# Kernel tuning notes

Hardware: AMD Instinct MI355X
Metric: run time of the kernel (lower is better)

## Reference

```python
import jax, jax.numpy as jnp
import numpy as np

B, T, C, HD = 4, 4096, 1024, 64  # batch, seq, n_embd, head_dim = n_embd//n_head


def setup_inputs() -> dict:
    key = jax.random.key(0)
    k1, k2, k3, k4 = jax.random.split(key, 4)
    scale = 0.02
    return {
        "x": jax.random.normal(k1, (B, T, C), dtype=jnp.float32),
        "Wq": jax.random.normal(k2, (C, HD), dtype=jnp.float32) * scale,
        "Wk": jax.random.normal(k3, (C, HD), dtype=jnp.float32) * scale,
        "Wv": jax.random.normal(k4, (C, HD), dtype=jnp.float32) * scale,
    }


def reference(x, Wq, Wk, Wv):
    # single-head projections: [B,T,C] @ [C,HD] -> [B,T,HD]
    q = jnp.einsum("btc,ch->bth", x, Wq)
    k = jnp.einsum("btc,ch->bth", x, Wk)
    v = jnp.einsum("btc,ch->bth", x, Wv)
    scale = k.shape[-1] ** -0.5
    # scores: [B,T,T], causal mask via -inf, stable softmax
    alpha = jnp.einsum("bqh,bkh->bqk", q, k) * scale
    t = x.shape[1]
    causal = jnp.tril(jnp.ones((t, t), dtype=bool))
    alpha = jnp.where(causal, alpha, -jnp.inf)
    alpha = jax.nn.softmax(alpha, axis=-1)
    # dropout p=0.0 -> identity
    h = jnp.einsum("bqk,bkh->bqh", alpha, v)
    return h
```

## Files before the change

### kernel.cpp

```cpp
#include <hip/hip_runtime.h>

#define T_SEQ 4096
#define C_DIM 1024
#define HD 64
#define NCH 272

typedef __attribute__((ext_vector_type(8))) __bf16 bf16x8;
typedef __attribute__((ext_vector_type(8))) unsigned short us8;
typedef __attribute__((ext_vector_type(4))) unsigned short us4;
typedef __attribute__((ext_vector_type(4))) float f32x4;
typedef __attribute__((ext_vector_type(16))) float f32x16;

#define QSCALE 0.18033688011112042f

__device__ __forceinline__ unsigned short f2bf(float f) {
    union { float f; unsigned u; } x; x.f = f;
    unsigned r = x.u + 0x7FFFu + ((x.u >> 16) & 1u);
    return (unsigned short)(r >> 16);
}

__device__ __forceinline__ float bf2f(unsigned short u) {
    union { unsigned u; float f; } x; x.u = ((unsigned)u) << 16;
    return x.f;
}

__device__ __forceinline__ us8 cvt8(float4 a, float4 b) {
    union { __bf16 h[8]; us8 v; } u;
    u.h[0] = (__bf16)a.x; u.h[1] = (__bf16)a.y; u.h[2] = (__bf16)a.z; u.h[3] = (__bf16)a.w;
    u.h[4] = (__bf16)b.x; u.h[5] = (__bf16)b.y; u.h[6] = (__bf16)b.z; u.h[7] = (__bf16)b.w;
    return u.v;
}

__device__ __forceinline__ us4 cvt4f(float a, float b, float c, float d) {
    union { __bf16 h[4]; us4 v; } u;
    u.h[0] = (__bf16)a; u.h[1] = (__bf16)b; u.h[2] = (__bf16)c; u.h[3] = (__bf16)d;
    return u.v;
}

__device__ __forceinline__ f32x16 zero16() {
    f32x16 v;
    #pragma unroll
    for (int j = 0; j < 16; ++j) v[j] = 0.f;
    return v;
}

__device__ __forceinline__ void gll16(const unsigned short* g, unsigned short* l) {
    __builtin_amdgcn_global_load_lds(
        (const __attribute__((address_space(1))) unsigned int*)g,
        (__attribute__((address_space(3))) unsigned int*)l,
        16, 0, 0);
}

__device__ __forceinline__ int swzs(int idx) {
    return idx ^ ((((idx) >> 6) & 7) << 3);
}

__device__ __forceinline__ int offf(int qt) {
    const int m = qt >> 1;
    return (qt & 1) ? (m + 1) * (m + 1) : m * m + m;
}

__global__ __launch_bounds__(256) void k_wtrans(const float* __restrict__ Wq,
                                                const float* __restrict__ Wk,
                                                const float* __restrict__ Wv,
                                                unsigned short* __restrict__ wt_g) {
    __shared__ unsigned short tile[64][72];
    const int bx = blockIdx.x;
    const int which = bx >> 4;
    const int kc = bx & 15;
    const int k0 = kc * 64;
    const float* W = (which == 0) ? Wq : ((which == 1) ? Wk : Wv);
    const int t = threadIdx.x;
    {
        const int r = t >> 2, c0 = (t & 3) * 16;
        const float4* src = reinterpret_cast<const float4*>(W + (k0 + r) * HD + c0);
        #pragma unroll
        for (int i = 0; i < 4; ++i) {
            float4 v = src[i];
            tile[r][c0 + 4 * i + 0] = f2bf(v.x);
            tile[r][c0 + 4 * i + 1] = f2bf(v.y);
            tile[r][c0 + 4 * i + 2] = f2bf(v.z);
            tile[r][c0 + 4 * i + 3] = f2bf(v.w);
        }
    }
    __syncthreads();
    {
        const int n = t >> 2, kc0 = (t & 3) * 16;
        alignas(16) unsigned short o[16];
        #pragma unroll
        for (int i = 0; i < 16; ++i) o[i] = tile[kc0 + i][n];
        const int row = which * 64 + n;
        const int g0 = kc0 >> 3;
        unsigned short* base = wt_g + (size_t)kc * 12288 + row * 64;
        *reinterpret_cast<us8*>(base + ((g0 ^ (row & 7)) << 3))       = *reinterpret_cast<const us8*>(&o[0]);
        *reinterpret_cast<us8*>(base + (((g0 + 1) ^ (row & 7)) << 3)) = *reinterpret_cast<const us8*>(&o[8]);
    }
}

__global__ __launch_bounds__(256) void k_proj(const float* __restrict__ x,
                                              const unsigned short* __restrict__ wt_g,
                                              unsigned short* __restrict__ qs,
                                              unsigned short* __restrict__ ksb,
                                              unsigned short* __restrict__ vt) {
    __shared__ unsigned short smem[29184];
    const int tid = threadIdx.x;
    const int w = tid >> 6, lane = tid & 63;
    const int l15 = lane & 15, g = lane >> 4;
    const int m0 = blockIdx.x * 32;
    const int sr = tid >> 3, sc0 = (tid & 7) * 8;
    const float* xrow = x + (size_t)(m0 + sr) * C_DIM + sc0;

    f32x4 acc[3][2];
    #pragma unroll
    for (int mf = 0; mf < 3; ++mf)
        #pragma unroll
        for (int nf = 0; nf < 2; ++nf)
            acc[mf][nf] = (f32x4){0.f, 0.f, 0.f, 0.f};

    {
        float4 xa = *reinterpret_cast<const float4*>(xrow);
        float4 xb = *reinterpret_cast<const float4*>(xrow + 4);
        *reinterpret_cast<us8*>(smem + sr * 72 + sc0) = cvt8(xa, xb);
        const unsigned short* wsrc = wt_g + w * 3072 + lane * 8;
        #pragma unroll
        for (int j = 0; j < 6; ++j)
            gll16(wsrc + j * 512, smem + 4608 + w * 3072 + j * 512);
    }
    __syncthreads();

    for (int kk = 0; kk < 16; ++kk) {
        const int cur = kk & 1;
        const int xb = cur * 2304,  xbn = (cur ^ 1) * 2304;
        const int wb = 4608 + cur * 12288, wbn = 4608 + (cur ^ 1) * 12288;
        float4 na, nb;
        if (kk < 15) {
            const unsigned short* wsrc = wt_g + (size_t)(kk + 1) * 12288 + w * 3072 + lane * 8;
            #pragma unroll
            for (int j = 0; j < 6; ++j)
                gll16(wsrc + j * 512, smem + wbn + w * 3072 + j * 512);
            na = *reinterpret_cast<const float4*>(xrow + (kk + 1) * 64);
            nb = *reinterpret_cast<const float4*>(xrow + (kk + 1) * 64 + 4);
        }
        #pragma unroll
        for (int k2 = 0; k2 < 2; ++k2) {
            bf16x8 bfr[2];
            #pragma unroll
            for (int nf = 0; nf < 2; ++nf)
                bfr[nf] = *reinterpret_cast<const bf16x8*>(
                    smem + xb + (nf * 16 + l15) * 72 + k2 * 32 + g * 8);
            #pragma unroll
            for (int mf = 0; mf < 3; ++mf) {
                bf16x8 afr = *reinterpret_cast<const bf16x8*>(
                    smem + wb + swzs(((3 * w + mf) * 16 + l15) * 64 + k2 * 32 + g * 8));
                #pragma unroll
                for (int nf = 0; nf < 2; ++nf)
                    acc[mf][nf] = __builtin_amdgcn_mfma_f32_16x16x32_bf16(
                        afr, bfr[nf], acc[mf][nf], 0, 0, 0);
            }
        }
        if (kk < 15)
            *reinterpret_cast<us8*>(smem + xbn + sr * 72 + sc0) = cvt8(na, nb);
        __syncthreads();
    }

    unsigned short* out_lds = smem;
    #pragma unroll
    for (int mf = 0; mf < 3; ++mf) {
        const int Mfr = 3 * w + mf;
        const float s = (Mfr < 4) ? QSCALE : 1.0f;
        #pragma unroll
        for (int nf = 0; nf < 2; ++nf) {
            union { __bf16 h[4]; us4 v; } u;
            #pragma unroll
            for (int r = 0; r < 4; ++r) u.h[r] = (__bf16)(acc[mf][nf][r] * s);
            *reinterpret_cast<us4*>(out_lds + (nf * 16 + l15) * 208 + Mfr * 16 + 4 * g) = u.v;
        }
    }
    __syncthreads();
    {
        const int r = tid >> 3, c = (tid & 7) * 8;
        const size_t gm = (size_t)(m0 + r);
        *reinterpret_cast<us8*>(qs + gm * 64 + c)  = *reinterpret_cast<const us8*>(out_lds + r * 208 + c);
        *reinterpret_cast<us8*>(ksb + gm * 64 + c) = *reinterpret_cast<const us8*>(out_lds + r * 208 + 64 + c);
    }
    {
        const int d = tid >> 2, j0 = (tid & 3) * 8;
        const int b = m0 >> 12, t0 = m0 & 4095;
        alignas(16) unsigned short tmp[8];
        #pragma unroll
        for (int j = 0; j < 8; ++j) tmp[j] = out_lds[(j0 + j) * 208 + 128 + d];
        *reinterpret_cast<us8*>(vt + (size_t)(b * 64 + d) * T_SEQ + t0 + j0) =
            *reinterpret_cast<const us8*>(tmp);
    }
}

__global__ __launch_bounds__(256) void k_attn(const unsigned short* __restrict__ qs,
                                              const unsigned short* __restrict__ ks,
                                              const unsigned short* __restrict__ vt,
                                              unsigned short* __restrict__ Opart,
                                              float* __restrict__ lw,
                                              float* __restrict__ out) {
    __shared__ unsigned short sm[16384];
    const int tid = threadIdx.x;
    const int w = tid >> 6, lane = tid & 63;
    const int l31 = lane & 31, hi = lane >> 5;
    const int batch = blockIdx.y;
    const int i = (NCH - 1) - blockIdx.x;
    int qt = min(31, (int)(2.0f * sqrtf((float)i)));
    while (offf(qt + 1) <= i) ++qt;
    while (offf(qt) > i) --qt;
    const int s = i - offf(qt);
    const int ns = (qt + 2) >> 1;
    const int it0 = s * 4;
    const int it1 = min(it0 + 4, 2 * qt + 2);
    const int qi = qt * 128 + 32 * w + l31;
    const size_t qrow = (size_t)batch * T_SEQ + qi;

    bf16x8 qf[4];
    #pragma unroll
    for (int df = 0; df < 4; ++df)
        qf[df] = *reinterpret_cast<const bf16x8*>(qs + qrow * 64 + df * 16 + hi * 8);

    f32x16 accO0 = zero16(), accO1 = zero16();
    float lp0 = 0.f, lp1 = 0.f, lp2 = 0.f, lp3 = 0.f;

    const int sr = tid >> 2, sc0 = (tid & 3) * 16;
    const unsigned short* kbase = ks + ((size_t)batch * T_SEQ + sr) * 64 + sc0;
    const unsigned short* vbase = vt + ((size_t)batch * 64 + sr) * T_SEQ + sc0;

    {
        us8 a0 = *reinterpret_cast<const us8*>(kbase + (size_t)it0 * 4096);
        us8 a1 = *reinterpret_cast<const us8*>(kbase + (size_t)it0 * 4096 + 8);
        us8 b0 = *reinterpret_cast<const us8*>(vbase + it0 * 64);
        us8 b1 = *reinterpret_cast<const us8*>(vbase + it0 * 64 + 8);
        us8 w0, w1;
        #pragma unroll
        for (int j = 0; j < 4; ++j) { w0[j] = b0[j]; w0[4 + j] = b1[j]; w1[j] = b0[4 + j]; w1[4 + j] = b1[4 + j]; }
        const int kd = sr * 64 + sc0, vd = 8192 + sr * 64 + sc0;
        *reinterpret_cast<us8*>(sm + swzs(kd))     = a0;
        *reinterpret_cast<us8*>(sm + swzs(kd + 8)) = a1;
        *reinterpret_cast<us8*>(sm + swzs(vd))     = w0;
        *reinterpret_cast<us8*>(sm + swzs(vd + 8)) = w1;
    }
    __syncthreads();

    for (int it = it0; it < it1; ++it) {
        const int cur = (it - it0) & 1;
        const bool pf = (it + 1 < it1);
        us8 n0, n1, m0, m1;
        if (pf) {
            n0 = *reinterpret_cast<const us8*>(kbase + (size_t)(it + 1) * 4096);
            n1 = *reinterpret_cast<const us8*>(kbase + (size_t)(it + 1) * 4096 + 8);
            m0 = *reinterpret_cast<const us8*>(vbase + (it + 1) * 64);
            m1 = *reinterpret_cast<const us8*>(vbase + (it + 1) * 64 + 8);
        }
        const int kb = cur * 4096;
        const int vb = 8192 + cur * 4096;
        const bool diag = (it >= 2 * qt);

        #pragma unroll
        for (int ksub = 0; ksub < 2; ++ksub) {
            f32x16 sv = zero16();
            __builtin_amdgcn_s_setprio(1);
            #pragma unroll
            for (int df = 0; df < 4; ++df) {
                bf16x8 afr = *reinterpret_cast<const bf16x8*>(
                    sm + swzs(kb + (ksub * 32 + l31) * 64 + df * 16 + hi * 8));
                sv = __builtin_amdgcn_mfma_f32_32x32x16_bf16(afr, qf[df], sv, 0, 0, 0);
            }
            __builtin_amdgcn_s_setprio(0);
            if (diag) {
                #pragma unroll
                for (int rr = 0; rr < 16; ++rr) {
                    const int kidx = it * 64 + ksub * 32 + (rr & 3) + 8 * (rr >> 2) + 4 * hi;
                    if (kidx > qi) sv[rr] = -1e30f;
                }
            }
            f32x16 pv;
            #pragma unroll
            for (int rr = 0; rr < 16; ++rr) pv[rr] = exp2f(sv[rr]);
            #pragma unroll
            for (int rr = 0; rr < 4; ++rr) {
                lp0 += pv[4 * rr + 0];
                lp1 += pv[4 * rr + 1];
                lp2 += pv[4 * rr + 2];
                lp3 += pv[4 * rr + 3];
            }
            us8 bfr0, bfr1;
            {
                us4 c0 = cvt4f(pv[0], pv[1], pv[2], pv[3]);
                us4 c1 = cvt4f(pv[4], pv[5], pv[6], pv[7]);
                us4 c2 = cvt4f(pv[8], pv[9], pv[10], pv[11]);
                us4 c3 = cvt4f(pv[12], pv[13], pv[14], pv[15]);
                #pragma unroll
                for (int j = 0; j < 4; ++j) {
                    bfr0[j] = c0[j]; bfr0[4 + j] = c1[j];
                    bfr1[j] = c2[j]; bfr1[4 + j] = c3[j];
                }
            }
            __builtin_amdgcn_s_setprio(1);
            {
                bf16x8 a00 = *reinterpret_cast<const bf16x8*>(
                    sm + swzs(vb + l31 * 64 + ksub * 32 + hi * 8));
                bf16x8 a01 = *reinterpret_cast<const bf16x8*>(
                    sm + swzs(vb + l31 * 64 + ksub * 32 + 16 + hi * 8));
                accO0 = __builtin_amdgcn_mfma_f32_32x32x16_bf16(
                    a00, *reinterpret_cast<bf16x8*>(&bfr0), accO0, 0, 0, 0);
                accO0 = __builtin_amdgcn_mfma_f32_32x32x16_bf16(
                    a01, *reinterpret_cast<bf16x8*>(&bfr1), accO0, 0, 0, 0);
                bf16x8 a10 = *reinterpret_cast<const bf16x8*>(
                    sm + swzs(vb + (32 + l31) * 64 + ksub * 32 + hi * 8));
                bf16x8 a11 = *reinterpret_cast<const bf16x8*>(
                    sm + swzs(vb + (32 + l31) * 64 + ksub * 32 + 16 + hi * 8));
                accO1 = __builtin_amdgcn_mfma_f32_32x32x16_bf16(
                    a10, *reinterpret_cast<bf16x8*>(&bfr0), accO1, 0, 0, 0);
                accO1 = __builtin_amdgcn_mfma_f32_32x32x16_bf16(
                    a11, *reinterpret_cast<bf16x8*>(&bfr1), accO1, 0, 0, 0);
            }
            __builtin_amdgcn_s_setprio(0);
        }
        if (pf) {
            us8 w0, w1;
            #pragma unroll
            for (int j = 0; j < 4; ++j) { w0[j] = m0[j]; w0[4 + j] = m1[j]; w1[j] = m0[4 + j]; w1[4 + j] = m1[4 + j]; }
            const int kd = (cur ^ 1) * 4096 + sr * 64 + sc0;
            const int vd = 8192 + (cur ^ 1) * 4096 + sr * 64 + sc0;
            *reinterpret_cast<us8*>(sm + swzs(kd))     = n0;
            *reinterpret_cast<us8*>(sm + swzs(kd + 8)) = n1;
            *reinterpret_cast<us8*>(sm + swzs(vd))     = w0;
            *reinterpret_cast<us8*>(sm + swzs(vd + 8)) = w1;
        }
        __syncthreads();
    }

    float l_run = (lp0 + lp1) + (lp2 + lp3);
    l_run += __shfl_xor(l_run, 32, 64);

    if (ns == 1) {
        const float inv = 1.0f / l_run;
        #pragma unroll
        for (int rg = 0; rg < 4; ++rg) {
            const int d0 = 4 * hi + 8 * rg;
            f32x4 o0 = {accO0[4 * rg] * inv, accO0[4 * rg + 1] * inv,
                        accO0[4 * rg + 2] * inv, accO0[4 * rg + 3] * inv};
            f32x4 o1 = {accO1[4 * rg] * inv, accO1[4 * rg + 1] * inv,
                        accO1[4 * rg + 2] * inv, accO1[4 * rg + 3] * inv};
            *reinterpret_cast<f32x4*>(out + qrow * 64 + d0)      = o0;
            *reinterpret_cast<f32x4*>(out + qrow * 64 + 32 + d0) = o1;
        }
    } else {
        const int pb = batch * NCH + i;
        const int q = 32 * w + l31;
        unsigned short* ob = Opart + (size_t)pb * 8192 + q * 64;
        #pragma unroll
        for (int rg = 0; rg < 4; ++rg) {
            const int d0 = 4 * hi + 8 * rg;
            *reinterpret_cast<us4*>(ob + d0) =
                cvt4f(accO0[4 * rg], accO0[4 * rg + 1], accO0[4 * rg + 2], accO0[4 * rg + 3]);
            *reinterpret_cast<us4*>(ob + 32 + d0) =
                cvt4f(accO1[4 * rg], accO1[4 * rg + 1], accO1[4 * rg + 2], accO1[4 * rg + 3]);
        }
        if (hi == 0) lw[(size_t)pb * 128 + q] = l_run;
    }
}

__global__ __launch_bounds__(256) void k_combine(const unsigned short* __restrict__ Opart,
                                                 const float* __restrict__ lw,
                                                 float* __restrict__ out) {
    const int qt = 2 + (blockIdx.x >> 1), half = blockIdx.x & 1;
    const int batch = blockIdx.y;
    const int t = threadIdx.x;
    const int q = half * 64 + (t >> 2), d0 = (t & 3) * 16;
    const int ns = (qt + 2) >> 1;
    const int pb0 = batch * NCH + offf(qt);
    float num[16];
    #pragma unroll
    for (int j = 0; j < 16; ++j) num[j] = 0.f;
    float lsum = 0.f;
    for (int s = 0; s < ns; ++s) {
        const int pb = pb0 + s;
        lsum += lw[(size_t)pb * 128 + q];
        const unsigned short* op = Opart + (size_t)pb * 8192 + q * 64 + d0;
        us8 v0 = *reinterpret_cast<const us8*>(op);
        us8 v1 = *reinterpret_cast<const us8*>(op + 8);
        #pragma unroll
        for (int j = 0; j < 8; ++j) {
            num[j] += bf2f(v0[j]);
            num[8 + j] += bf2f(v1[j]);
        }
    }
    const float inv = 1.f / lsum;
    float* o = out + ((size_t)batch * T_SEQ + qt * 128 + q) * 64 + d0;
    #pragma unroll
    for (int h = 0; h < 4; ++h) {
        f32x4 v = {num[4 * h] * inv, num[4 * h + 1] * inv,
                   num[4 * h + 2] * inv, num[4 * h + 3] * inv};
        *reinterpret_cast<f32x4*>(o + 4 * h) = v;
    }
}

extern "C" void kernel_launch(void* const* d_in, const int* in_sizes, int n_in,
                              void* d_out, int out_size, void* d_ws, size_t ws_size,
                              hipStream_t stream) {
    (void)in_sizes; (void)n_in; (void)out_size; (void)ws_size;
    const float* x  = (const float*)d_in[0];
    const float* Wq = (const float*)d_in[1];
    const float* Wk = (const float*)d_in[2];
    const float* Wv = (const float*)d_in[3];
    float* out = (float*)d_out;
    unsigned short* ws16 = (unsigned short*)d_ws;
    unsigned short* wt_g  = ws16;
    unsigned short* qsb   = ws16 + 196608;
    unsigned short* ksb   = qsb + 1048576;
    unsigned short* vtb   = ksb + 1048576;
    unsigned short* Opart = vtb + 1048576;
    float* lw = (float*)(Opart + 8912896);
    k_wtrans <<<dim3(48),      dim3(256), 0, stream>>>(Wq, Wk, Wv, wt_g);
    k_proj   <<<dim3(512),     dim3(256), 0, stream>>>(x, wt_g, qsb, ksb, vtb);
    k_attn   <<<dim3(NCH, 4),  dim3(256), 0, stream>>>(qsb, ksb, vtb, Opart, lw, out);
    k_combine<<<dim3(60, 4),   dim3(256), 0, stream>>>(Opart, lw, out);
}
```

Before: 62.57 us.

## Enlarge projection tile to 64 rows and 128-wide K steps with 512 threads

The QKV projection kernel now processes 64 token rows per block with 8 waves split 2x4 over rows and output columns. Each K step is widened to 128 channels, which halves the loop trip count and the number of barriers. The transposed weight buffer is re-laid out in 128-wide chunks with a matching swizzle. The aim is to halve the per-block weight reloads through LDS and improve reuse, at the cost of far more shared memory (about 130 KB), which lowers occupancy, and half as many blocks.

Result: faster. 61.32 us (-2.0%).

```diff
diff --git a/kernel.cpp b/kernel.cpp
--- a/kernel.cpp
+++ b/kernel.cpp
@@ -53,6 +53,9 @@
 
 __device__ __forceinline__ int swzs(int idx) {
     return idx ^ ((((idx) >> 6) & 7) << 3);
+}
+__device__ __forceinline__ int swzw(int idx) {
+    return idx ^ ((((idx) >> 7) & 7) << 3);
 }
 
 __device__ __forceinline__ int offf(int qt) {
@@ -90,24 +93,26 @@
         #pragma unroll
         for (int i = 0; i < 16; ++i) o[i] = tile[kc0 + i][n];
         const int row = which * 64 + n;
-        const int g0 = kc0 >> 3;
-        unsigned short* base = wt_g + (size_t)kc * 12288 + row * 64;
+        const int c8 = kc >> 1;
+        const int g0 = ((kc & 1) * 64 + kc0) >> 3;
+        unsigned short* base = wt_g + (size_t)c8 * 24576 + row * 128;
         *reinterpret_cast<us8*>(base + ((g0 ^ (row & 7)) << 3))       = *reinterpret_cast<const us8*>(&o[0]);
         *reinterpret_cast<us8*>(base + (((g0 + 1) ^ (row & 7)) << 3)) = *reinterpret_cast<const us8*>(&o[8]);
     }
 }
 
-__global__ __launch_bounds__(256) void k_proj(const float* __restrict__ x,
+__global__ __launch_bounds__(512) void k_proj(const float* __restrict__ x,
                                               const unsigned short* __restrict__ wt_g,
                                               unsigned short* __restrict__ qs,
                                               unsigned short* __restrict__ ksb,
                                               unsigned short* __restrict__ vt) {
-    __shared__ unsigned short smem[29184];
+    __shared__ unsigned short smem[66560];
     const int tid = threadIdx.x;
     const int w = tid >> 6, lane = tid & 63;
     const int l15 = lane & 15, g = lane >> 4;
-    const int m0 = blockIdx.x * 32;
-    const int sr = tid >> 3, sc0 = (tid & 7) * 8;
+    const int wm = w & 1, wn = w >> 1;
+    const int m0 = blockIdx.x * 64;
+    const int sr = tid >> 3, sc0 = (tid & 7) * 16;
     const float* xrow = x + (size_t)(m0 + sr) * C_DIM + sc0;
 
     f32x4 acc[3][2];
@@ -118,62 +123,70 @@
             acc[mf][nf] = (f32x4){0.f, 0.f, 0.f, 0.f};
 
     {
-        float4 xa = *reinterpret_cast<const float4*>(xrow);
-        float4 xb = *reinterpret_cast<const float4*>(xrow + 4);
-        *reinterpret_cast<us8*>(smem + sr * 72 + sc0) = cvt8(xa, xb);
+        float4 a0 = *reinterpret_cast<const float4*>(xrow);
+        float4 a1 = *reinterpret_cast<const float4*>(xrow + 4);
+        float4 a2 = *reinterpret_cast<const float4*>(xrow + 8);
+        float4 a3 = *reinterpret_cast<const float4*>(xrow + 12);
+        *reinterpret_cast<us8*>(smem + sr * 136 + sc0)     = cvt8(a0, a1);
+        *reinterpret_cast<us8*>(smem + sr * 136 + sc0 + 8) = cvt8(a2, a3);
         const unsigned short* wsrc = wt_g + w * 3072 + lane * 8;
         #pragma unroll
         for (int j = 0; j < 6; ++j)
-            gll16(wsrc + j * 512, smem + 4608 + w * 3072 + j * 512);
+            gll16(wsrc + j * 512, smem + 17408 + w * 3072 + j * 512);
     }
     __syncthreads();
 
-    for (int kk = 0; kk < 16; ++kk) {
+    for (int kk = 0; kk < 8; ++kk) {
         const int cur = kk & 1;
-        const int xb = cur * 2304,  xbn = (cur ^ 1) * 2304;
-        const int wb = 4608 + cur * 12288, wbn = 4608 + (cur ^ 1) * 12288;
-        float4 na, nb;
-        if (kk < 15) {
-            const unsigned short* wsrc = wt_g + (size_t)(kk + 1) * 12288 + w * 3072 + lane * 8;
+        const int xb = cur * 8704,  xbn = (cur ^ 1) * 8704;
+        const int wb = 17408 + cur * 24576, wbn = 17408 + (cur ^ 1) * 24576;
+        float4 n0, n1, n2, n3;
+        if (kk < 7) {
+            const unsigned short* wsrc = wt_g + (size_t)(kk + 1) * 24576 + w * 3072 + lane * 8;
             #pragma unroll
             for (int j = 0; j < 6; ++j)
                 gll16(wsrc + j * 512, smem + wbn + w * 3072 + j * 512);
-            na = *reinterpret_cast<const float4*>(xrow + (kk + 1) * 64);
-            nb = *reinterpret_cast<const float4*>(xrow + (kk + 1) * 64 + 4);
-        }
-        #pragma unroll
-        for (int k2 = 0; k2 < 2; ++k2) {
+            n0 = *reinterpret_cast<const float4*>(xrow + (kk + 1) * 128);
+            n1 = *reinterpret_cast<const float4*>(xrow + (kk + 1) * 128 + 4);
+            n2 = *reinterpret_cast<const float4*>(xrow + (kk + 1) * 128 + 8);
+            n3 = *reinterpret_cast<const float4*>(xrow + (kk + 1) * 128 + 12);
+        }
+        #pragma unroll
+        for (int k2 = 0; k2 < 4; ++k2) {
             bf16x8 bfr[2];
             #pragma unroll
             for (int nf = 0; nf < 2; ++nf)
                 bfr[nf] = *reinterpret_cast<const bf16x8*>(
-                    smem + xb + (nf * 16 + l15) * 72 + k2 * 32 + g * 8);
+                    smem + xb + (wm * 32 + nf * 16 + l15) * 136 + k2 * 32 + g * 8);
             #pragma unroll
             for (int mf = 0; mf < 3; ++mf) {
                 bf16x8 afr = *reinterpret_cast<const bf16x8*>(
-                    smem + wb + swzs(((3 * w + mf) * 16 + l15) * 64 + k2 * 32 + g * 8));
+                    smem + wb + swzw(((3 * wn + mf) * 16 + l15) * 128 + k2 * 32 + g * 8));
                 #pragma unroll
                 for (int nf = 0; nf < 2; ++nf)
                     acc[mf][nf] = __builtin_amdgcn_mfma_f32_16x16x32_bf16(
                         afr, bfr[nf], acc[mf][nf], 0, 0, 0);
             }
         }
-        if (kk < 15)
-            *reinterpret_cast<us8*>(smem + xbn + sr * 72 + sc0) = cvt8(na, nb);
+        if (kk < 7) {
+            *reinterpret_cast<us8*>(smem + xbn + sr * 136 + sc0)     = cvt8(n0, n1);
+            *reinterpret_cast<us8*>(smem + xbn + sr * 136 + sc0 + 8) = cvt8(n2, n3);
+        }
         __syncthreads();
     }
 
     unsigned short* out_lds = smem;
     #pragma unroll
     for (int mf = 0; mf < 3; ++mf) {
-        const int Mfr = 3 * w + mf;
+        const int Mfr = 3 * wn + mf;
         const float s = (Mfr < 4) ? QSCALE : 1.0f;
         #pragma unroll
         for (int nf = 0; nf < 2; ++nf) {
             union { __bf16 h[4]; us4 v; } u;
             #pragma unroll
             for (int r = 0; r < 4; ++r) u.h[r] = (__bf16)(acc[mf][nf][r] * s);
-            *reinterpret_cast<us4*>(out_lds + (nf * 16 + l15) * 208 + Mfr * 16 + 4 * g) = u.v;
+            *reinterpret_cast<us4*>(
+                out_lds + (wm * 32 + nf * 16 + l15) * 208 + Mfr * 16 + 4 * g) = u.v;
         }
     }
     __syncthreads();
@@ -184,7 +197,7 @@
         *reinterpret_cast<us8*>(ksb + gm * 64 + c) = *reinterpret_cast<const us8*>(out_lds + r * 208 + 64 + c);
     }
     {
-        const int d = tid >> 2, j0 = (tid & 3) * 8;
+        const int d = tid >> 3, j0 = (tid & 7) * 8;
         const int b = m0 >> 12, t0 = m0 & 4095;
         alignas(16) unsigned short tmp[8];
         #pragma unroll
@@ -416,7 +429,7 @@
     unsigned short* Opart = vtb + 1048576;
     float* lw = (float*)(Opart + 8912896);
     k_wtrans <<<dim3(48),      dim3(256), 0, stream>>>(Wq, Wk, Wv, wt_g);
-    k_proj   <<<dim3(512),     dim3(256), 0, stream>>>(x, wt_g, qsb, ksb, vtb);
+    k_proj   <<<dim3(256),     dim3(512), 0, stream>>>(x, wt_g, qsb, ksb, vtb);
     k_attn   <<<dim3(NCH, 4),  dim3(256), 0, stream>>>(qsb, ksb, vtb, Opart, lw, out);
     k_combine<<<dim3(60, 4),   dim3(256), 0, stream>>>(Opart, lw, out);
 }
```
